# Performance work log

Hardware: AMD Instinct MI355X
Metric: run time of the kernel (lower is better)

The kernel has to match this reference:

```python
import jax, jax.numpy as jnp
import numpy as np
import math

B, S, D = 32, 2048, 1024


def setup_inputs() -> dict:
    key = jax.random.key(0)
    ks = jax.random.split(key, 8)
    x = jax.random.normal(ks[0], (B, S, D), dtype=jnp.float32)
    # right-padding mask: True = padding, each row has a random valid length in [S//2, S]
    lengths = jax.random.randint(ks[1], (B, 1), S // 2, S + 1)
    attention_mask = jnp.arange(S)[None, :] >= lengths  # [B, S] bool
    scale = 1.0 / math.sqrt(D)
    gate_w1 = jax.random.normal(ks[2], (D, D // 2), dtype=jnp.float32) * scale
    gate_b1 = jnp.zeros((D // 2,), dtype=jnp.float32)
    gate_w2 = jax.random.normal(ks[3], (D // 2, 1), dtype=jnp.float32) * scale
    gate_b2 = jnp.zeros((1,), dtype=jnp.float32)
    decay_lambda = jnp.float32(0.05)
    attention_query = jax.random.normal(ks[4], (D,), dtype=jnp.float32)
    key_w = jax.random.normal(ks[5], (D, D), dtype=jnp.float32) * scale
    key_b = jnp.zeros((D,), dtype=jnp.float32)
    return {
        "utterance_embeddings": x,
        "attention_mask": attention_mask,
        "gate_w1": gate_w1, "gate_b1": gate_b1,
        "gate_w2": gate_w2, "gate_b2": gate_b2,
        "decay_lambda": decay_lambda,
        "attention_query": attention_query,
        "key_w": key_w, "key_b": key_b,
    }


def reference(utterance_embeddings, attention_mask, gate_w1, gate_b1, gate_w2,
              gate_b2, decay_lambda, attention_query, key_w, key_b):
    x = utterance_embeddings  # [B, S, D]
    bsz, seq_len, dim = x.shape
    # suppression gate: Linear -> GELU(exact) -> Linear -> Sigmoid, output [B, S, 1]
    h = jax.nn.gelu(jnp.einsum('bsd,dk->bsk', x, gate_w1) + gate_b1, approximate=False)
    gate = jax.nn.sigmoid(jnp.einsum('bsk,ko->bso', h, gate_w2) + gate_b2)
    gated = x * gate  # [B, S, D]
    keys = jnp.einsum('bsd,de->bse', gated, key_w) + key_b  # [B, S, D]
    logits = jnp.einsum('d,bsd->bs', attention_query, keys) / jnp.sqrt(jnp.float32(dim))
    t_idx = jnp.arange(seq_len, dtype=jnp.float32)[None, :]  # [1, S]
    valid_lengths = jnp.sum(~attention_mask, axis=1, keepdims=True).astype(jnp.float32)
    penalty_idx = jnp.maximum(valid_lengths - 1.0 - t_idx, 0.0)  # [B, S]
    pos_lambda = jax.nn.softplus(decay_lambda)
    decayed = logits - pos_lambda * penalty_idx
    decayed = jnp.where(attention_mask, jnp.float32(-10000.0), decayed)
    alpha = jax.nn.softmax(decayed, axis=1)  # [B, S]
    scene_vector = jnp.einsum('bs,bsd->bd', alpha, gated)  # [B, D]
    return scene_vector
```

## Files before the change

kernel.cpp:

```cpp
#include <hip/hip_runtime.h>
#include <hip/hip_bf16.h>
#include <math.h>

#define BQ 32
#define SQ 2048
#define DQ 1024
#define NQ 512
#define MQ (BQ*SQ)
#define SS 16
#define BM 128
#define BN 256
#define BK 32

typedef __attribute__((ext_vector_type(8))) short bf16x8;
typedef __attribute__((ext_vector_type(4))) float f32x4;

__device__ __forceinline__ short f2bf(float f){
  return __builtin_bit_cast(short, __float2bfloat16(f));
}

__device__ __forceinline__ void gload_lds16(const void* g, void* l){
  __builtin_amdgcn_global_load_lds(
      (const __attribute__((address_space(1))) unsigned int*)g,
      (__attribute__((address_space(3))) unsigned int*)l, 16, 0, 0);
}

__global__ void k_w1t(const float* __restrict__ w1, short* __restrict__ w1t){
  int i = blockIdx.x*256 + threadIdx.x;
  if (i >= NQ*DQ) return;
  int n = i >> 10, k = i & (DQ-1);
  w1t[i] = f2bf(w1[(size_t)k*NQ + n]);
}

__global__ void k_wq(const float* __restrict__ kw, const float* __restrict__ kb,
                     const float* __restrict__ q, float* __restrict__ wq){
  __shared__ float sh[4];
  int d = blockIdx.x, t = threadIdx.x;
  const float* row = (d < DQ) ? (kw + (size_t)d*DQ) : kb;
  float s = 0.f;
  for (int e=t;e<DQ;e+=256) s += row[e]*q[e];
  #pragma unroll
  for (int o=32;o;o>>=1) s += __shfl_down(s,o);
  if ((t&63)==0) sh[t>>6]=s;
  __syncthreads();
  if (t==0) wq[d] = sh[0]+sh[1]+sh[2]+sh[3];
}

__global__ void k_det(const unsigned int* __restrict__ m, int* __restrict__ flag){
  __shared__ int so, sf;
  int t = threadIdx.x;
  if (t==0){ so=0; sf=0; }
  __syncthreads();
  int o=0, f1=0;
  for (int i=t;i<MQ/4;i+=256){
    unsigned v = m[i];
    if (v==0x3F800000u) f1=1;
    else if (v>1u) o=1;
  }
  if (o) atomicOr(&so,1);
  if (f1) atomicOr(&sf,1);
  __syncthreads();
  if (t==0) *flag = so?2:(sf?1:0);
}

__global__ __launch_bounds__(512) void k_gate(
    const float* __restrict__ x, const short* __restrict__ w1t,
    const float* __restrict__ wq, const float* __restrict__ w2,
    const float* __restrict__ b1,
    float* __restrict__ gpart, float* __restrict__ xq)
{
  __shared__ __align__(16) short As[2][BM*BK];
  __shared__ __align__(16) short Bs[2][BN*BK];
  __shared__ float wqs[DQ];

  int tid = threadIdx.x;
  int phys = blockIdx.x;
  int bid = ((phys & 7) << 7) | (phys >> 3);
  int bm = bid >> 1, bn = bid & 1;
  int m0 = bm*BM;
  int lane = tid & 63, wid = tid >> 6;
  int wm = wid >> 2, wn = wid & 3;
  int lo = lane & 15, hi = lane >> 4;

  wqs[tid]     = wq[tid];
  wqs[tid+512] = wq[tid+512];

  int ar = tid >> 2, ac = (tid & 3) * 8;
  const float* asrc = x + (size_t)(m0 + ar)*DQ + ac;
  const short* bsrc = w1t + (size_t)(bn*BN + (tid>>2))*DQ + (tid&3)*8;

  float w2v[4], b1v[4];
  #pragma unroll
  for (int fn=0;fn<4;fn++){
    int n = bn*BN + wn*64 + fn*16 + lo;
    w2v[fn] = w2[n]; b1v[fn] = b1[n];
  }

  f32x4 r0 = *(const f32x4*)(asrc);
  f32x4 r1 = *(const f32x4*)(asrc + 4);
  gload_lds16(bsrc,                    &Bs[0][tid*8]);
  gload_lds16(bsrc + (size_t)128*DQ,   &Bs[0][tid*8 + 4096]);
  __syncthreads();
  float xqacc = 0.f;
  {
    if (bn == 0){
      f32x4 w0 = *(const f32x4*)(wqs + ac);
      f32x4 w1v = *(const f32x4*)(wqs + ac + 4);
      #pragma unroll
      for (int j=0;j<4;j++)
        xqacc += r0[j]*w0[j] + r1[j]*w1v[j];
    }
    bf16x8 s0;
    #pragma unroll
    for (int j=0;j<4;j++){ s0[j]=f2bf(r0[j]); s0[4+j]=f2bf(r1[j]); }
    *(bf16x8*)(&As[0][ar*BK + ac]) = s0;
  }
  __syncthreads();

  f32x4 acc[4][4];
  #pragma unroll
  for (int a=0;a<4;a++)
    #pragma unroll
    for (int b=0;b<4;b++) acc[a][b] = (f32x4){0.f,0.f,0.f,0.f};

  for (int t=0;t<32;t++){
    int cur = t & 1, nxt = cur ^ 1;
    int k0n = (t+1)*BK;
    if (t < 31){
      r0 = *(const f32x4*)(asrc + k0n);
      r1 = *(const f32x4*)(asrc + k0n + 4);
      gload_lds16(bsrc + k0n,                  &Bs[nxt][tid*8]);
      gload_lds16(bsrc + (size_t)128*DQ + k0n, &Bs[nxt][tid*8 + 4096]);
    }
    bf16x8 af[4], bfr[4];
    #pragma unroll
    for (int fm=0;fm<4;fm++)
      af[fm] = *(const bf16x8*)(&As[cur][(wm*64+fm*16+lo)*BK + hi*8]);
    #pragma unroll
    for (int fn=0;fn<4;fn++)
      bfr[fn] = *(const bf16x8*)(&Bs[cur][(wn*64+fn*16+lo)*BK + hi*8]);
    #pragma unroll
    for (int fm=0;fm<4;fm++)
      #pragma unroll
      for (int fn=0;fn<4;fn++)
        acc[fm][fn] = __builtin_amdgcn_mfma_f32_16x16x32_bf16(af[fm], bfr[fn], acc[fm][fn], 0,0,0);
    if (t < 31){
      if (bn == 0){
        f32x4 w0 = *(const f32x4*)(wqs + k0n + ac);
        f32x4 w1v = *(const f32x4*)(wqs + k0n + ac + 4);
        #pragma unroll
        for (int j=0;j<4;j++)
          xqacc += r0[j]*w0[j] + r1[j]*w1v[j];
      }
      bf16x8 s0;
      #pragma unroll
      for (int j=0;j<4;j++){ s0[j]=f2bf(r0[j]); s0[4+j]=f2bf(r1[j]); }
      *(bf16x8*)(&As[nxt][ar*BK + ac]) = s0;
    }
    __syncthreads();
  }

  if (bn == 0){
    float s = xqacc;
    s += __shfl_xor(s, 1);
    s += __shfl_xor(s, 2);
    if ((tid & 3) == 0) xq[m0 + ar] = s;
  }

  #pragma unroll
  for (int fm=0;fm<4;fm++){
    #pragma unroll
    for (int j=0;j<4;j++){
      float s = 0.f;
      #pragma unroll
      for (int fn=0;fn<4;fn++){
        float h = acc[fm][fn][j] + b1v[fn];
        float g = 0.5f*h*(1.0f + erff(h*0.70710678118f));
        s += g*w2v[fn];
      }
      s += __shfl_xor(s,1); s += __shfl_xor(s,2);
      s += __shfl_xor(s,4); s += __shfl_xor(s,8);
      if (lo == 0){
        int p = bn*4 + wn;
        gpart[(size_t)p*MQ + m0 + wm*64 + fm*16 + hi*4 + j] = s;
      }
    }
  }
}

__device__ __forceinline__ float bredsum(float v, float* sh){
  #pragma unroll
  for (int o=32;o;o>>=1) v += __shfl_down(v,o);
  __syncthreads();
  if ((threadIdx.x&63)==0) sh[threadIdx.x>>6]=v;
  __syncthreads();
  return sh[0]+sh[1]+sh[2]+sh[3];
}
__device__ __forceinline__ float bredmax(float v, float* sh){
  #pragma unroll
  for (int o=32;o;o>>=1) v = fmaxf(v,__shfl_down(v,o));
  __syncthreads();
  if ((threadIdx.x&63)==0) sh[threadIdx.x>>6]=v;
  __syncthreads();
  return fmaxf(fmaxf(sh[0],sh[1]),fmaxf(sh[2],sh[3]));
}

__global__ __launch_bounds__(256) void k_soft(
    const void* __restrict__ maskp, const int* __restrict__ flag,
    const float* __restrict__ gpart, const float* __restrict__ xqv,
    const float* __restrict__ wq, const float* __restrict__ lamp,
    const float* __restrict__ b2, float* __restrict__ wgt)
{
  __shared__ float sh[4];
  int b = blockIdx.x, t = threadIdx.x;
  int fl = *flag;
  const unsigned char* m8 = (const unsigned char*)maskp;
  const float* mf = (const float*)maskp;
  const int* mi = (const int*)maskp;
  size_t base = (size_t)b*SQ;
  int cnt = 0;
  int msk[8];
  #pragma unroll
  for (int i=0;i<8;i++){
    int s = t + i*256;
    size_t idx = base + s;
    int mm = (fl==2) ? (m8[idx]!=0) : (fl==1) ? (mf[idx]!=0.0f) : (mi[idx]!=0);
    msk[i]=mm; cnt += mm^1;
  }
  float L = bredsum((float)cnt, sh);
  float qb = wq[DQ];
  float lam = lamp[0];
  float posl = fmaxf(lam,0.f) + log1pf(expf(-fabsf(lam)));
  const float inv = 0.03125f;
  float dec[8], gt[8];
  float mx = -3.0e38f;
  float b2v = b2[0];
  #pragma unroll
  for (int i=0;i<8;i++){
    int s = t + i*256;
    size_t r = base + s;
    float gsum = b2v;
    #pragma unroll
    for (int p=0;p<8;p++) gsum += gpart[(size_t)p*MQ + r];
    float gate = 1.0f/(1.0f+expf(-gsum));
    gt[i] = gate;
    float lg = (gate*xqv[r] + qb)*inv;
    float pen = fmaxf(L - 1.0f - (float)s, 0.0f);
    float d = lg - posl*pen;
    if (msk[i]) d = -10000.0f;
    dec[i]=d; mx = fmaxf(mx,d);
  }
  mx = bredmax(mx, sh);
  float ssum = 0.f;
  #pragma unroll
  for (int i=0;i<8;i++){ dec[i] = expf(dec[i]-mx); ssum += dec[i]; }
  ssum = bredsum(ssum, sh);
  float rinv = 1.0f/ssum;
  #pragma unroll
  for (int i=0;i<8;i++){
    size_t r = base + t + i*256;
    wgt[r] = dec[i]*rinv*gt[i];
  }
}

__global__ __launch_bounds__(256) void k_pool(
    const float* __restrict__ x, const float* __restrict__ wgt,
    float* __restrict__ part)
{
  int b = blockIdx.x, sc = blockIdx.y, t = threadIdx.x;
  const int SCH = SQ/SS;
  const float* xb = x + ((size_t)b*SQ + (size_t)sc*SCH)*DQ + t*4;
  const float* wb = wgt + (size_t)b*SQ + (size_t)sc*SCH;
  f32x4 a = {0.f,0.f,0.f,0.f};
  #pragma unroll 4
  for (int s=0;s<SCH;s++){
    float w = wb[s];
    f32x4 v = *(const f32x4*)(xb + (size_t)s*DQ);
    a[0] += w*v[0]; a[1] += w*v[1]; a[2] += w*v[2]; a[3] += w*v[3];
  }
  *(f32x4*)(part + ((size_t)sc*BQ + b)*DQ + t*4) = a;
}

__global__ __launch_bounds__(256) void k_fin(const float* __restrict__ part, float* __restrict__ out){
  int i = blockIdx.x*256 + threadIdx.x;
  float s = 0.f;
  #pragma unroll
  for (int c=0;c<SS;c++) s += part[(size_t)c*(BQ*DQ) + i];
  out[i]=s;
}

extern "C" void kernel_launch(void* const* d_in, const int* in_sizes, int n_in,
                              void* d_out, int out_size, void* d_ws, size_t ws_size,
                              hipStream_t stream)
{
  const float* x    = (const float*)d_in[0];
  const void*  mask = d_in[1];
  const float* w1   = (const float*)d_in[2];
  const float* b1   = (const float*)d_in[3];
  const float* w2   = (const float*)d_in[4];
  const float* b2   = (const float*)d_in[5];
  const float* lam  = (const float*)d_in[6];
  const float* q    = (const float*)d_in[7];
  const float* kw   = (const float*)d_in[8];
  const float* kb   = (const float*)d_in[9];
  char* ws = (char*)d_ws;
  short* w1t = (short*)ws;
  float* wq  = (float*)(ws + (1<<20));
  int* flag  = (int*)(ws + (1<<20) + 8192);
  float* gpart = (float*)(ws + (1<<20) + 16384);
  float* xq  = gpart + 8*MQ;
  float* wgt = xq + MQ;
  float* part= wgt + MQ;
  float* out = (float*)d_out;

  k_w1t<<<dim3((NQ*DQ+255)/256), 256, 0, stream>>>(w1, w1t);
  k_wq<<<dim3(DQ+1), 256, 0, stream>>>(kw, kb, q, wq);
  k_det<<<dim3(1), 256, 0, stream>>>((const unsigned int*)mask, flag);
  k_gate<<<dim3((MQ/BM)*2), 512, 0, stream>>>(x, w1t, wq, w2, b1, gpart, xq);
  k_soft<<<dim3(BQ), 256, 0, stream>>>(mask, flag, gpart, xq, wq, lam, b2, wgt);
  k_pool<<<dim3(BQ, SS), 256, 0, stream>>>(x, wgt, part);
  k_fin<<<dim3((BQ*DQ)/256), 256, 0, stream>>>(part, out);
}
```

Baseline: 197.4 us.

## Fuse gate, softmax weighting and pooling into one GEMM kernel

The gate kernel now takes 64-row tiles covering the full N=512 hidden width, so each block finishes the full gate sum in shared memory. It then computes unnormalized softmax weights without a max subtraction and pools its x tile directly while that tile is likely still in cache. Per-block exp sums are written out, and a final kernel reduces the partials and divides by the denominator. This removes the gpart/xq/wgt round trips, the separate softmax and pool kernels, and a second full read of x from HBM. The cost is halved M tiles, which lowers MFMA reuse of B, and skipping the max shift risks overflow for large logits.

Result: faster. 185.3 us (-6.1%).

```diff
diff --git a/kernel.cpp b/kernel.cpp
--- a/kernel.cpp
+++ b/kernel.cpp
@@ -7,12 +7,12 @@
 #define DQ 1024
 #define NQ 512
 #define MQ (BQ*SQ)
-#define SS 16
-#define BM 128
-#define BN 256
+#define BM 64
+#define BN 512
 #define BK 32
 
 typedef __attribute__((ext_vector_type(8))) short bf16x8;
+typedef __attribute__((ext_vector_type(4))) short bf16x4;
 typedef __attribute__((ext_vector_type(4))) float f32x4;
 
 __device__ __forceinline__ short f2bf(float f){
@@ -63,57 +63,82 @@
   if (t==0) *flag = so?2:(sf?1:0);
 }
 
+__global__ __launch_bounds__(256) void k_len(const void* __restrict__ maskp,
+                                             const int* __restrict__ flag,
+                                             int* __restrict__ lens){
+  __shared__ int sh[4];
+  int b = blockIdx.x, t = threadIdx.x;
+  int fl = *flag;
+  const unsigned char* m8 = (const unsigned char*)maskp;
+  const float* mf = (const float*)maskp;
+  const int* mi = (const int*)maskp;
+  int cnt = 0;
+  #pragma unroll
+  for (int i=0;i<8;i++){
+    size_t idx = (size_t)b*SQ + t + i*256;
+    int mm = (fl==2) ? (m8[idx]!=0) : (fl==1) ? (mf[idx]!=0.0f) : (mi[idx]!=0);
+    cnt += mm^1;
+  }
+  #pragma unroll
+  for (int o=32;o;o>>=1) cnt += __shfl_down(cnt,o);
+  if ((t&63)==0) sh[t>>6]=cnt;
+  __syncthreads();
+  if (t==0) lens[b] = sh[0]+sh[1]+sh[2]+sh[3];
+}
+
 __global__ __launch_bounds__(512) void k_gate(
     const float* __restrict__ x, const short* __restrict__ w1t,
     const float* __restrict__ wq, const float* __restrict__ w2,
-    const float* __restrict__ b1,
-    float* __restrict__ gpart, float* __restrict__ xq)
+    const float* __restrict__ b1, const float* __restrict__ b2p,
+    const float* __restrict__ lamp,
+    const void* __restrict__ maskp, const int* __restrict__ flag,
+    const int* __restrict__ lens,
+    float* __restrict__ part, float* __restrict__ wsum)
 {
   __shared__ __align__(16) short As[2][BM*BK];
   __shared__ __align__(16) short Bs[2][BN*BK];
   __shared__ float wqs[DQ];
+  __shared__ float red[8][BM];
+  __shared__ float wrow[BM];
+  __shared__ float xqrow[BM];
 
   int tid = threadIdx.x;
-  int phys = blockIdx.x;
-  int bid = ((phys & 7) << 7) | (phys >> 3);
-  int bm = bid >> 1, bn = bid & 1;
+  int bm = blockIdx.x;
   int m0 = bm*BM;
+  int batch = bm >> 5;
+  int s0 = (bm & 31) * 64;
   int lane = tid & 63, wid = tid >> 6;
-  int wm = wid >> 2, wn = wid & 3;
+  int wn = wid;
   int lo = lane & 15, hi = lane >> 4;
 
   wqs[tid]     = wq[tid];
   wqs[tid+512] = wq[tid+512];
 
-  int ar = tid >> 2, ac = (tid & 3) * 8;
+  int ar = tid >> 3, ac = (tid & 7) * 4;
   const float* asrc = x + (size_t)(m0 + ar)*DQ + ac;
-  const short* bsrc = w1t + (size_t)(bn*BN + (tid>>2))*DQ + (tid&3)*8;
+  const short* bsrc = w1t + (size_t)(tid>>2)*DQ + (tid&3)*8;
 
   float w2v[4], b1v[4];
   #pragma unroll
   for (int fn=0;fn<4;fn++){
-    int n = bn*BN + wn*64 + fn*16 + lo;
+    int n = wn*64 + fn*16 + lo;
     w2v[fn] = w2[n]; b1v[fn] = b1[n];
   }
 
   f32x4 r0 = *(const f32x4*)(asrc);
-  f32x4 r1 = *(const f32x4*)(asrc + 4);
-  gload_lds16(bsrc,                    &Bs[0][tid*8]);
-  gload_lds16(bsrc + (size_t)128*DQ,   &Bs[0][tid*8 + 4096]);
+  #pragma unroll
+  for (int i=0;i<4;i++)
+    gload_lds16(bsrc + (size_t)i*128*DQ, &Bs[0][i*4096 + tid*8]);
   __syncthreads();
   float xqacc = 0.f;
   {
-    if (bn == 0){
-      f32x4 w0 = *(const f32x4*)(wqs + ac);
-      f32x4 w1v = *(const f32x4*)(wqs + ac + 4);
-      #pragma unroll
-      for (int j=0;j<4;j++)
-        xqacc += r0[j]*w0[j] + r1[j]*w1v[j];
-    }
-    bf16x8 s0;
-    #pragma unroll
-    for (int j=0;j<4;j++){ s0[j]=f2bf(r0[j]); s0[4+j]=f2bf(r1[j]); }
-    *(bf16x8*)(&As[0][ar*BK + ac]) = s0;
+    f32x4 w0 = *(const f32x4*)(wqs + ac);
+    #pragma unroll
+    for (int j=0;j<4;j++) xqacc += r0[j]*w0[j];
+    bf16x4 s0v;
+    #pragma unroll
+    for (int j=0;j<4;j++) s0v[j]=f2bf(r0[j]);
+    *(bf16x4*)(&As[0][ar*BK + ac]) = s0v;
   }
   __syncthreads();
 
@@ -128,14 +153,14 @@
     int k0n = (t+1)*BK;
     if (t < 31){
       r0 = *(const f32x4*)(asrc + k0n);
-      r1 = *(const f32x4*)(asrc + k0n + 4);
-      gload_lds16(bsrc + k0n,                  &Bs[nxt][tid*8]);
-      gload_lds16(bsrc + (size_t)128*DQ + k0n, &Bs[nxt][tid*8 + 4096]);
+      #pragma unroll
+      for (int i=0;i<4;i++)
+        gload_lds16(bsrc + (size_t)i*128*DQ + k0n, &Bs[nxt][i*4096 + tid*8]);
     }
     bf16x8 af[4], bfr[4];
     #pragma unroll
     for (int fm=0;fm<4;fm++)
-      af[fm] = *(const bf16x8*)(&As[cur][(wm*64+fm*16+lo)*BK + hi*8]);
+      af[fm] = *(const bf16x8*)(&As[cur][(fm*16+lo)*BK + hi*8]);
     #pragma unroll
     for (int fn=0;fn<4;fn++)
       bfr[fn] = *(const bf16x8*)(&Bs[cur][(wn*64+fn*16+lo)*BK + hi*8]);
@@ -145,26 +170,21 @@
       for (int fn=0;fn<4;fn++)
         acc[fm][fn] = __builtin_amdgcn_mfma_f32_16x16x32_bf16(af[fm], bfr[fn], acc[fm][fn], 0,0,0);
     if (t < 31){
-      if (bn == 0){
-        f32x4 w0 = *(const f32x4*)(wqs + k0n + ac);
-        f32x4 w1v = *(const f32x4*)(wqs + k0n + ac + 4);
-        #pragma unroll
-        for (int j=0;j<4;j++)
-          xqacc += r0[j]*w0[j] + r1[j]*w1v[j];
-      }
-      bf16x8 s0;
-      #pragma unroll
-      for (int j=0;j<4;j++){ s0[j]=f2bf(r0[j]); s0[4+j]=f2bf(r1[j]); }
-      *(bf16x8*)(&As[nxt][ar*BK + ac]) = s0;
+      f32x4 w0 = *(const f32x4*)(wqs + k0n + ac);
+      #pragma unroll
+      for (int j=0;j<4;j++) xqacc += r0[j]*w0[j];
+      bf16x4 s0v;
+      #pragma unroll
+      for (int j=0;j<4;j++) s0v[j]=f2bf(r0[j]);
+      *(bf16x4*)(&As[nxt][ar*BK + ac]) = s0v;
     }
     __syncthreads();
   }
 
-  if (bn == 0){
+  {
     float s = xqacc;
-    s += __shfl_xor(s, 1);
-    s += __shfl_xor(s, 2);
-    if ((tid & 3) == 0) xq[m0 + ar] = s;
+    s += __shfl_xor(s,1); s += __shfl_xor(s,2); s += __shfl_xor(s,4);
+    if ((tid & 7) == 0) xqrow[ar] = s;
   }
 
   #pragma unroll
@@ -180,113 +200,63 @@
       }
       s += __shfl_xor(s,1); s += __shfl_xor(s,2);
       s += __shfl_xor(s,4); s += __shfl_xor(s,8);
-      if (lo == 0){
-        int p = bn*4 + wn;
-        gpart[(size_t)p*MQ + m0 + wm*64 + fm*16 + hi*4 + j] = s;
-      }
-    }
-  }
-}
-
-__device__ __forceinline__ float bredsum(float v, float* sh){
-  #pragma unroll
-  for (int o=32;o;o>>=1) v += __shfl_down(v,o);
-  __syncthreads();
-  if ((threadIdx.x&63)==0) sh[threadIdx.x>>6]=v;
-  __syncthreads();
-  return sh[0]+sh[1]+sh[2]+sh[3];
-}
-__device__ __forceinline__ float bredmax(float v, float* sh){
-  #pragma unroll
-  for (int o=32;o;o>>=1) v = fmaxf(v,__shfl_down(v,o));
-  __syncthreads();
-  if ((threadIdx.x&63)==0) sh[threadIdx.x>>6]=v;
-  __syncthreads();
-  return fmaxf(fmaxf(sh[0],sh[1]),fmaxf(sh[2],sh[3]));
-}
-
-__global__ __launch_bounds__(256) void k_soft(
-    const void* __restrict__ maskp, const int* __restrict__ flag,
-    const float* __restrict__ gpart, const float* __restrict__ xqv,
-    const float* __restrict__ wq, const float* __restrict__ lamp,
-    const float* __restrict__ b2, float* __restrict__ wgt)
-{
-  __shared__ float sh[4];
-  int b = blockIdx.x, t = threadIdx.x;
-  int fl = *flag;
-  const unsigned char* m8 = (const unsigned char*)maskp;
-  const float* mf = (const float*)maskp;
-  const int* mi = (const int*)maskp;
-  size_t base = (size_t)b*SQ;
-  int cnt = 0;
-  int msk[8];
-  #pragma unroll
-  for (int i=0;i<8;i++){
-    int s = t + i*256;
-    size_t idx = base + s;
-    int mm = (fl==2) ? (m8[idx]!=0) : (fl==1) ? (mf[idx]!=0.0f) : (mi[idx]!=0);
-    msk[i]=mm; cnt += mm^1;
-  }
-  float L = bredsum((float)cnt, sh);
-  float qb = wq[DQ];
-  float lam = lamp[0];
-  float posl = fmaxf(lam,0.f) + log1pf(expf(-fabsf(lam)));
-  const float inv = 0.03125f;
-  float dec[8], gt[8];
-  float mx = -3.0e38f;
-  float b2v = b2[0];
-  #pragma unroll
-  for (int i=0;i<8;i++){
-    int s = t + i*256;
-    size_t r = base + s;
-    float gsum = b2v;
-    #pragma unroll
-    for (int p=0;p<8;p++) gsum += gpart[(size_t)p*MQ + r];
+      if (lo == 0) red[wid][fm*16 + hi*4 + j] = s;
+    }
+  }
+  __syncthreads();
+
+  if (tid < 64){
+    int s = s0 + tid;
+    float gsum = b2p[0];
+    #pragma unroll
+    for (int w=0;w<8;w++) gsum += red[w][tid];
     float gate = 1.0f/(1.0f+expf(-gsum));
-    gt[i] = gate;
-    float lg = (gate*xqv[r] + qb)*inv;
-    float pen = fmaxf(L - 1.0f - (float)s, 0.0f);
-    float d = lg - posl*pen;
-    if (msk[i]) d = -10000.0f;
-    dec[i]=d; mx = fmaxf(mx,d);
-  }
-  mx = bredmax(mx, sh);
-  float ssum = 0.f;
-  #pragma unroll
-  for (int i=0;i<8;i++){ dec[i] = expf(dec[i]-mx); ssum += dec[i]; }
-  ssum = bredsum(ssum, sh);
-  float rinv = 1.0f/ssum;
-  #pragma unroll
-  for (int i=0;i<8;i++){
-    size_t r = base + t + i*256;
-    wgt[r] = dec[i]*rinv*gt[i];
-  }
-}
-
-__global__ __launch_bounds__(256) void k_pool(
-    const float* __restrict__ x, const float* __restrict__ wgt,
-    float* __restrict__ part)
-{
-  int b = blockIdx.x, sc = blockIdx.y, t = threadIdx.x;
-  const int SCH = SQ/SS;
-  const float* xb = x + ((size_t)b*SQ + (size_t)sc*SCH)*DQ + t*4;
-  const float* wb = wgt + (size_t)b*SQ + (size_t)sc*SCH;
-  f32x4 a = {0.f,0.f,0.f,0.f};
-  #pragma unroll 4
-  for (int s=0;s<SCH;s++){
-    float w = wb[s];
-    f32x4 v = *(const f32x4*)(xb + (size_t)s*DQ);
-    a[0] += w*v[0]; a[1] += w*v[1]; a[2] += w*v[2]; a[3] += w*v[3];
-  }
-  *(f32x4*)(part + ((size_t)sc*BQ + b)*DQ + t*4) = a;
-}
-
-__global__ __launch_bounds__(256) void k_fin(const float* __restrict__ part, float* __restrict__ out){
+    float qb = wq[DQ];
+    float lg = (gate*xqrow[tid] + qb)*0.03125f;
+    float lam = lamp[0];
+    float posl = fmaxf(lam,0.f) + log1pf(expf(-fabsf(lam)));
+    int L = lens[batch];
+    float pen = fmaxf((float)L - 1.0f - (float)s, 0.0f);
+    int fl = *flag;
+    size_t mi_ = (size_t)batch*SQ + s;
+    int mm = (fl==2) ? (((const unsigned char*)maskp)[mi_]!=0)
+           : (fl==1) ? (((const float*)maskp)[mi_]!=0.0f)
+                     : (((const int*)maskp)[mi_]!=0);
+    float e = mm ? 0.0f : expf(lg - posl*pen);
+    wrow[tid] = e*gate;
+    float tsum = e;
+    #pragma unroll
+    for (int o=1;o<64;o<<=1) tsum += __shfl_xor(tsum,o);
+    if (tid==0) wsum[bm] = tsum;
+  }
+  __syncthreads();
+
+  {
+    int d0 = tid*2;
+    const float* xb = x + (size_t)m0*DQ + d0;
+    float a0=0.f, a1=0.f;
+    #pragma unroll 8
+    for (int s=0;s<64;s++){
+      float w = wrow[s];
+      float2 v = *(const float2*)(xb + (size_t)s*DQ);
+      a0 += w*v.x; a1 += w*v.y;
+    }
+    *(float2*)(part + (size_t)bm*DQ + d0) = make_float2(a0,a1);
+  }
+}
+
+__global__ __launch_bounds__(256) void k_fin(const float* __restrict__ part,
+                                             const float* __restrict__ wsum,
+                                             float* __restrict__ out){
   int i = blockIdx.x*256 + threadIdx.x;
+  int b = i >> 10, d = i & 1023;
+  float den = 0.f;
+  #pragma unroll
+  for (int c=0;c<32;c++) den += wsum[b*32+c];
   float s = 0.f;
   #pragma unroll
-  for (int c=0;c<SS;c++) s += part[(size_t)c*(BQ*DQ) + i];
-  out[i]=s;
+  for (int c=0;c<32;c++) s += part[((size_t)(b*32+c))*DQ + d];
+  out[i] = s/den;
 }
 
 extern "C" void kernel_launch(void* const* d_in, const int* in_sizes, int n_in,
@@ -307,17 +277,16 @@
   short* w1t = (short*)ws;
   float* wq  = (float*)(ws + (1<<20));
   int* flag  = (int*)(ws + (1<<20) + 8192);
-  float* gpart = (float*)(ws + (1<<20) + 16384);
-  float* xq  = gpart + 8*MQ;
-  float* wgt = xq + MQ;
-  float* part= wgt + MQ;
+  int* lens  = (int*)(ws + (1<<20) + 8448);
+  float* wsum= (float*)(ws + (1<<20) + 12544);
+  float* part= (float*)(ws + (1<<20) + 20736);
   float* out = (float*)d_out;
 
   k_w1t<<<dim3((NQ*DQ+255)/256), 256, 0, stream>>>(w1, w1t);
   k_wq<<<dim3(DQ+1), 256, 0, stream>>>(kw, kb, q, wq);
   k_det<<<dim3(1), 256, 0, stream>>>((const unsigned int*)mask, flag);
-  k_gate<<<dim3((MQ/BM)*2), 512, 0, stream>>>(x, w1t, wq, w2, b1, gpart, xq);
-  k_soft<<<dim3(BQ), 256, 0, stream>>>(mask, flag, gpart, xq, wq, lam, b2, wgt);
-  k_pool<<<dim3(BQ, SS), 256, 0, stream>>>(x, wgt, part);
-  k_fin<<<dim3((BQ*DQ)/256), 256, 0, stream>>>(part, out);
-}
+  k_len<<<dim3(BQ), 256, 0, stream>>>(mask, flag, lens);
+  k_gate<<<dim3(MQ/BM), 512, 0, stream>>>(x, w1t, wq, w2, b1, b2, lam,
+                                          mask, flag, lens, part, wsum);
+  k_fin<<<dim3((BQ*DQ)/256), 256, 0, stream>>>(part, wsum, out);
+}
```
